# Performance work log

Hardware: AMD Instinct MI355X
Metric: run time of the kernel (lower is better)

## Reference

```python
import jax, jax.numpy as jnp
import numpy as np

S, N, H, E, V = 64, 256, 1024, 256, 128  # seq_len, batch, hidden, embed, vocab
DIR = 2  # bidirectional encoder


def setup_inputs() -> dict:
    key = jax.random.key(0)
    ks = jax.random.split(key, 16)
    sd = lambda fan: 1.0 / np.sqrt(fan)
    inp = {
        'x': jax.random.randint(ks[0], (N,), 0, V),
        'encoder_states': jax.random.normal(ks[1], (S, N, DIR * H), dtype=jnp.float32),
        'hidden': jax.random.normal(ks[2], (2, N, H), dtype=jnp.float32),
        'cell': jnp.zeros((2, N, H), dtype=jnp.float32),
        'emb': jax.random.normal(ks[3], (V, E), dtype=jnp.float32),
        'U_w': jax.random.normal(ks[4], (H, DIR * H), dtype=jnp.float32) * sd(DIR * H),
        'U_b': jnp.zeros((H,), jnp.float32),
        'W_w': jax.random.normal(ks[5], (H, H), dtype=jnp.float32) * sd(H),
        'W_b': jnp.zeros((H,), jnp.float32),
        'attn_w': jax.random.normal(ks[6], (1, H), dtype=jnp.float32) * sd(H),
        'attn_b': jnp.zeros((1,), jnp.float32),
        'W_ih0': jax.random.normal(ks[7], (3 * H, DIR * H + E), dtype=jnp.float32) * sd(H),
        'W_hh0': jax.random.normal(ks[8], (3 * H, H), dtype=jnp.float32) * sd(H),
        'b_ih0': jnp.zeros((3 * H,), jnp.float32),
        'b_hh0': jnp.zeros((3 * H,), jnp.float32),
        'W_ih1': jax.random.normal(ks[9], (3 * H, H), dtype=jnp.float32) * sd(H),
        'W_hh1': jax.random.normal(ks[10], (3 * H, H), dtype=jnp.float32) * sd(H),
        'b_ih1': jnp.zeros((3 * H,), jnp.float32),
        'b_hh1': jnp.zeros((3 * H,), jnp.float32),
        'fc_w': jax.random.normal(ks[11], (V, H), dtype=jnp.float32) * sd(H),
        'fc_b': jnp.zeros((V,), jnp.float32),
    }
    return inp


def _gru_cell(x, h, W_ih, W_hh, b_ih, b_hh):
    # PyTorch GRU cell math. x:(N,Din), h:(N,H) -> (N,H)
    gi = x @ W_ih.T + b_ih
    gh = h @ W_hh.T + b_hh
    ir, iz, i_n = jnp.split(gi, 3, axis=-1)
    hr, hz, h_n = jnp.split(gh, 3, axis=-1)
    r = jax.nn.sigmoid(ir + hr)
    z = jax.nn.sigmoid(iz + hz)
    n = jnp.tanh(i_n + r * h_n)
    return (1.0 - z) * n + z * h


def reference(x, encoder_states, hidden, cell, emb, U_w, U_b, W_w, W_b,
              attn_w, attn_b, W_ih0, W_hh0, b_ih0, b_hh0,
              W_ih1, W_hh1, b_ih1, b_hh1, fc_w, fc_b):
    # embedding (dropout is identity at inference)
    emb_x = emb[x]                                   # (N, E)
    # additive (Bahdanau) attention
    u = jnp.einsum('snd,hd->snh', encoder_states, U_w) + U_b   # (S,N,H)
    w = hidden[-1] @ W_w.T + W_b                                # (N,H)
    energy = jnp.tanh(u + w[None]) @ attn_w.T + attn_b          # (S,N,1)
    attention = jax.nn.softmax(energy, axis=0)                  # softmax over seq dim
    context = jnp.einsum('sn,snd->nd', attention[..., 0], encoder_states)  # (N, 2H)
    rnn_input = jnp.concatenate([context, emb_x], axis=-1)      # (N, 2H+E)
    # 2-layer single-step GRU (inter-layer dropout = identity at inference)
    h0 = _gru_cell(rnn_input, hidden[0], W_ih0, W_hh0, b_ih0, b_hh0)
    h1 = _gru_cell(h0, hidden[1], W_ih1, W_hh1, b_ih1, b_hh1)
    hidden_new = jnp.stack([h0, h1], axis=0)                    # (2, N, H)
    predictions = h1 @ fc_w.T + fc_b                            # (N, V)
    return predictions, hidden_new, attention
```

## Files before the change

kernel.cpp:

```cpp
#include <hip/hip_runtime.h>
#include <stdint.h>

typedef __attribute__((ext_vector_type(8))) short bf16x8;
typedef __attribute__((ext_vector_type(4))) float f32x4;
typedef __attribute__((ext_vector_type(8))) int i32x8;

#define DEVI __device__ __forceinline__

DEVI unsigned short f2bf(float f) {
    union { float f; uint32_t u; } v; v.f = f;
    uint32_t r = v.u + 0x7FFFu + ((v.u >> 16) & 1u);
    return (unsigned short)(r >> 16);
}
DEVI float bf2f(unsigned short h) {
    union { uint32_t u; float f; } v; v.u = ((uint32_t)h) << 16;
    return v.f;
}
DEVI bf16x8 pack8(float4 a, float4 b) {
    bf16x8 o;
    o[0]=(short)f2bf(a.x); o[1]=(short)f2bf(a.y); o[2]=(short)f2bf(a.z); o[3]=(short)f2bf(a.w);
    o[4]=(short)f2bf(b.x); o[5]=(short)f2bf(b.y); o[6]=(short)f2bf(b.z); o[7]=(short)f2bf(b.w);
    return o;
}

DEVI unsigned char f2e4m3(float x) {
    union { float f; uint32_t u; } v; v.f = x;
    uint32_t sign = (v.u >> 24) & 0x80u;
    v.u &= 0x7FFFFFFFu;
    if (v.f >= 464.f) return (unsigned char)(sign | 0x7Eu);
    if (v.f < 0.0009765625f) return (unsigned char)sign;
    uint32_t e = v.u >> 23;
    float q = __builtin_rintf(v.f * 512.f);
    uint32_t ms = (uint32_t)q;
    uint32_t subres = sign | (ms >= 8u ? 0x08u : ms);
    uint32_t r = v.u + 0x7FFFFu + ((v.u >> 20) & 1u);
    uint32_t er = r >> 23;
    uint32_t normres = (er > 135u) ? (sign | 0x7Eu)
                                   : (sign | ((er - 120u) << 3) | ((r >> 20) & 7u));
    return (unsigned char)((e < 121u) ? subres : normres);
}

DEVI float e4m3f(unsigned char u) {
    union { uint32_t u; float f; } v;
    v.u = (((uint32_t)u & 0x80u) << 24) | (((uint32_t)u & 0x7Fu) << 20);
    return v.f * 0x1p120f;
}

#define GLOAD_LDS16(gsrc, ldst) \
    __builtin_amdgcn_global_load_lds((__attribute__((address_space(1))) void*)(gsrc), \
                                     (__attribute__((address_space(3))) void*)(ldst), 16, 0, 0)

#define BARR asm volatile("s_barrier" ::: "memory")
#define WAITV(n) asm volatile("s_waitcnt vmcnt(" #n ")" ::: "memory")

__global__ void k_prep(const float* __restrict__ es, const float* __restrict__ U_w,
                       const float* __restrict__ W_w, const float* __restrict__ fc_w,
                       const float* __restrict__ hidden,
                       const float* __restrict__ Wih0, const float* __restrict__ Whh0,
                       const float* __restrict__ Wih1, const float* __restrict__ Whh1,
                       unsigned char* __restrict__ ES_F8, unsigned char* __restrict__ UW_F8,
                       unsigned short* __restrict__ WW_BF, unsigned short* __restrict__ FCW_BF,
                       unsigned short* __restrict__ A0, unsigned short* __restrict__ A1,
                       unsigned short* __restrict__ H1B,
                       unsigned short* __restrict__ B0, unsigned short* __restrict__ B1) {
    int i = blockIdx.x * blockDim.x + threadIdx.x;
    const int S0 = 4194304, S1 = S0 + 262144, S2 = S1 + 131072, S3 = S2 + 16384;
    const int S4 = S3 + 32768, S5 = S4 + 1703936, S6 = S5 + 1048576;
    if (i < S0) {
        const float4* s = (const float4*)(es + (size_t)i * 8);
        float4 a = s[0], b = s[1];
        float vv[8] = {a.x, a.y, a.z, a.w, b.x, b.y, b.z, b.w};
        unsigned long long p8 = 0;
        #pragma unroll
        for (int k = 0; k < 8; ++k) p8 |= (unsigned long long)f2e4m3(vv[k]) << (8 * k);
        *(unsigned long long*)(ES_F8 + (size_t)i * 8) = p8;
    } else if (i < S1) {
        int j = i - S0;
        const float4* s = (const float4*)(U_w + (size_t)j * 8);
        float4 a = s[0], b = s[1];
        float vv[8] = {a.x, a.y, a.z, a.w, b.x, b.y, b.z, b.w};
        unsigned long long p8 = 0;
        #pragma unroll
        for (int k = 0; k < 8; ++k) p8 |= (unsigned long long)f2e4m3(vv[k] * 16.f) << (8 * k);
        *(unsigned long long*)(UW_F8 + (size_t)j * 8) = p8;
    } else if (i < S2) {
        int j = i - S1;
        const float4* s = (const float4*)(W_w + (size_t)j * 8);
        *(bf16x8*)(WW_BF + (size_t)j * 8) = pack8(s[0], s[1]);
    } else if (i < S3) {
        int j = i - S2;
        const float4* s = (const float4*)(fc_w + (size_t)j * 8);
        *(bf16x8*)(FCW_BF + (size_t)j * 8) = pack8(s[0], s[1]);
    } else if (i < S4) {
        int j = i - S3;
        int n = j >> 7, e0 = (j & 127) * 8;
        const float4* p0 = (const float4*)(hidden + (size_t)n * 1024 + e0);
        const float4* p1 = (const float4*)(hidden + 262144 + (size_t)n * 1024 + e0);
        bf16x8 o0 = pack8(p0[0], p0[1]);
        bf16x8 o1 = pack8(p1[0], p1[1]);
        *(bf16x8*)(A0 + (size_t)n * 3328 + 2304 + e0) = o0;
        *(bf16x8*)(A1 + (size_t)n * 2048 + 1024 + e0) = o1;
        *(bf16x8*)(H1B + (size_t)n * 1024 + e0) = o1;
    } else if (i < S5) {
        unsigned j = (unsigned)(i - S4);
        unsigned r = j / 416u;
        int kc = (int)(j - r * 416u) * 8;
        const float* src = nullptr;
        if (r < 2048)      src = (kc < 2304) ? (Wih0 + (size_t)r * 2304 + kc)
                                             : (Whh0 + (size_t)r * 1024 + (kc - 2304));
        else if (r < 3072) { if (kc < 2304)  src = Wih0 + (size_t)r * 2304 + kc; }
        else               { if (kc >= 2304) src = Whh0 + (size_t)(r - 1024) * 1024 + (kc - 2304); }
        bf16x8 o;
        if (src) { const float4* s4 = (const float4*)src; o = pack8(s4[0], s4[1]); }
        else     { for (int k = 0; k < 8; ++k) o[k] = 0; }
        *(bf16x8*)(B0 + (size_t)r * 3328 + kc) = o;
    } else if (i < S6) {
        int j = i - S5;
        int r = j >> 8;
        int kc = (j & 255) * 8;
        const float* src = nullptr;
        if (r < 2048)      src = (kc < 1024) ? (Wih1 + (size_t)r * 1024 + kc)
                                             : (Whh1 + (size_t)r * 1024 + (kc - 1024));
        else if (r < 3072) { if (kc < 1024)  src = Wih1 + (size_t)r * 1024 + kc; }
        else               { if (kc >= 1024) src = Whh1 + (size_t)(r - 1024) * 1024 + (kc - 1024); }
        bf16x8 o;
        if (src) { const float4* s4 = (const float4*)src; o = pack8(s4[0], s4[1]); }
        else     { for (int k = 0; k < 8; ++k) o[k] = 0; }
        *(bf16x8*)(B1 + (size_t)r * 2048 + kc) = o;
    }
}

__global__ __launch_bounds__(256) void gemm_bt_sk2(
        const unsigned short* __restrict__ A, const unsigned short* __restrict__ B,
        float* __restrict__ Cpart, int K, int ksl) {
    __shared__ __align__(16) char lds[65536];
    const int NTT = ksl >> 6;

    const int t = threadIdx.x;
    const int w = t >> 6, lane = t & 63;
    const int wm = w >> 1, wn = w & 1;
    const int lg = lane >> 4, r16 = lane & 15;
    const int z = blockIdx.z;
    const int nbx = gridDim.x;
    const int N = nbx * 128, M = gridDim.y * 128;

    int d = blockIdx.y * nbx + blockIdx.x;
    int f = d;
    int nwg = nbx * gridDim.y;
    if ((nwg & 7) == 0) { int cpx = nwg >> 3; f = (d & 7) * cpx + (d >> 3); }
    const int bx = f % nbx, by = f / nbx;
    const int row0 = by * 128, col0 = bx * 128;

    const unsigned short* gsrc[8];
    unsigned lodst[8];
    #pragma unroll
    for (int q = 0; q < 8; ++q) {
        int isB = q >> 2, rq = q & 3;
        int row = rq * 32 + w * 8 + (lane >> 3);
        int slot = (lane & 7) ^ (lane >> 3);
        gsrc[q] = (isB ? B + (size_t)(col0 + row) * K
                       : A + (size_t)(row0 + row) * K) + (size_t)z * ksl + slot * 8;
        lodst[q] = (unsigned)(isB * 16384 + (rq * 32 + w * 8) * 128);
    }

#define STAGE(T) do { \
    char* lp_ = lds + ((T) & 1) * 32768; \
    _Pragma("unroll") \
    for (int q_ = 0; q_ < 8; ++q_) \
        GLOAD_LDS16(gsrc[q_] + (size_t)(T) * 64, lp_ + lodst[q_]); \
} while (0)

    const unsigned swz = (unsigned)((r16 & 7) << 4);
    unsigned aoff[4], boff[4];
    #pragma unroll
    for (int m = 0; m < 4; ++m)
        aoff[m] = ((unsigned)((wm * 64 + m * 16 + r16) * 128 + lg * 16)) ^ swz;
    #pragma unroll
    for (int n = 0; n < 4; ++n)
        boff[n] = 16384u + (((unsigned)((wn * 64 + n * 16 + r16) * 128 + lg * 16)) ^ swz);

    f32x4 acc[4][4];
    #pragma unroll
    for (int m = 0; m < 4; ++m)
        #pragma unroll
        for (int n = 0; n < 4; ++n)
            #pragma unroll
            for (int q = 0; q < 4; ++q) acc[m][n][q] = 0.0f;

    STAGE(0);
    #pragma unroll 1
    for (int tt = 0; tt < NTT; ++tt) {
        if (tt + 1 < NTT) { STAGE(tt + 1); WAITV(8); }
        else              { WAITV(0); }
        BARR;
        const char* lp = lds + (tt & 1) * 32768;
        #pragma unroll
        for (int kk = 0; kk < 2; ++kk) {
            bf16x8 afr[4], bfr[4];
            #pragma unroll
            for (int n = 0; n < 4; ++n) bfr[n] = *(const bf16x8*)(lp + (boff[n] ^ (kk << 6)));
            #pragma unroll
            for (int m = 0; m < 4; ++m) afr[m] = *(const bf16x8*)(lp + (aoff[m] ^ (kk << 6)));
            #pragma unroll
            for (int m = 0; m < 4; ++m)
                #pragma unroll
                for (int n = 0; n < 4; ++n)
                    acc[m][n] = __builtin_amdgcn_mfma_f32_16x16x32_bf16(
                        afr[m], bfr[n], acc[m][n], 0, 0, 0);
        }
        BARR;
    }
#undef STAGE

    float* Cz = Cpart + (size_t)z * (size_t)M * N;
    #pragma unroll
    for (int m = 0; m < 4; ++m)
        #pragma unroll
        for (int n = 0; n < 4; ++n)
            #pragma unroll
            for (int q = 0; q < 4; ++q) {
                int row = row0 + wm * 64 + m * 16 + lg * 4 + q;
                int col = col0 + wn * 64 + n * 16 + r16;
                Cz[(size_t)row * N + col] = acc[m][n][q];
            }
}

__global__ __launch_bounds__(256) void gemm_energy128_f8(
        const unsigned char* __restrict__ A, const unsigned char* __restrict__ B,
        const float* __restrict__ attn_w, const float* __restrict__ U_b,
        const float* __restrict__ W_b, const float* __restrict__ WP,
        float* __restrict__ e_part) {
    const int NTT = 16;
    __shared__ __align__(16) char lds[65536];

    const int t = threadIdx.x;
    const int w = t >> 6, lane = t & 63;
    const int wm = w >> 1, wn = w & 1;
    const int lg = lane >> 4, r16 = lane & 15;

    int d = blockIdx.y * gridDim.x + blockIdx.x;
    int f = (d & 7) * 128 + (d >> 3);
    const int bx = f & 7, by = f >> 3;
    const int row0 = by * 128, col0 = bx * 128;

    const unsigned char* gsrc[8];
    unsigned lodst[8];
    #pragma unroll
    for (int q = 0; q < 8; ++q) {
        int isB = q >> 2, rq = q & 3;
        int row = rq * 32 + w * 8 + (lane >> 3);
        int slot = (lane & 7) ^ (lane >> 3);
        gsrc[q] = (isB ? B + (size_t)(col0 + row) * 2048
                       : A + (size_t)(row0 + row) * 2048) + slot * 16;
        lodst[q] = (unsigned)(isB * 16384 + (rq * 32 + w * 8) * 128);
    }

#define STAGE(T) do { \
    char* lp_ = lds + ((T) & 1) * 32768; \
    _Pragma("unroll") \
    for (int q_ = 0; q_ < 8; ++q_) \
        GLOAD_LDS16(gsrc[q_] + (size_t)(T) * 128, lp_ + lodst[q_]); \
} while (0)

    unsigned s16[2];
    #pragma unroll
    for (int sel = 0; sel < 2; ++sel)
        s16[sel] = (unsigned)(((sel * 4 + lg) ^ (r16 & 7)) << 4);
    unsigned arow[4], brow[4];
    #pragma unroll
    for (int m = 0; m < 4; ++m) arow[m] = (unsigned)((wm * 64 + m * 16 + r16) * 128);
    #pragma unroll
    for (int n = 0; n < 4; ++n) brow[n] = 16384u + (unsigned)((wn * 64 + n * 16 + r16) * 128);

    f32x4 acc[4][4];
    #pragma unroll
    for (int m = 0; m < 4; ++m)
        #pragma unroll
        for (int n = 0; n < 4; ++n)
            #pragma unroll
            for (int q = 0; q < 4; ++q) acc[m][n][q] = 0.0f;

    STAGE(0);
    #pragma unroll 1
    for (int tt = 0; tt < NTT; ++tt) {
        if (tt + 1 < NTT) { STAGE(tt + 1); WAITV(8); }
        else              { WAITV(0); }
        BARR;
        const char* lp = lds + (tt & 1) * 32768;
        i32x8 a8[4], b8[4];
        #pragma unroll
        for (int n = 0; n < 4; ++n) {
            int4 lo = *(const int4*)(lp + brow[n] + s16[0]);
            int4 hi = *(const int4*)(lp + brow[n] + s16[1]);
            b8[n] = (i32x8){lo.x, lo.y, lo.z, lo.w, hi.x, hi.y, hi.z, hi.w};
        }
        #pragma unroll
        for (int m = 0; m < 4; ++m) {
            int4 lo = *(const int4*)(lp + arow[m] + s16[0]);
            int4 hi = *(const int4*)(lp + arow[m] + s16[1]);
            a8[m] = (i32x8){lo.x, lo.y, lo.z, lo.w, hi.x, hi.y, hi.z, hi.w};
        }
        #pragma unroll
        for (int m = 0; m < 4; ++m)
            #pragma unroll
            for (int n = 0; n < 4; ++n)
                acc[m][n] = __builtin_amdgcn_mfma_scale_f32_16x16x128_f8f6f4(
                    a8[m], b8[n], acc[m][n], 0, 0,
                    0, 0x7F7F7F7F, 0, 0x7F7F7F7F);
        BARR;
    }
#undef STAGE

    float aw[4], ub[4];
    #pragma unroll
    for (int n = 0; n < 4; ++n) {
        int col = col0 + wn * 64 + n * 16 + r16;
        aw[n] = attn_w[col];
        ub[n] = U_b[col] + W_b[col];
    }
    #pragma unroll
    for (int m = 0; m < 4; ++m)
        #pragma unroll
        for (int q = 0; q < 4; ++q) {
            int row = row0 + wm * 64 + m * 16 + lg * 4 + q;
            const float* wrow = WP + (size_t)(row & 255) * 1024;
            float e = 0.f;
            #pragma unroll
            for (int n = 0; n < 4; ++n) {
                int col = col0 + wn * 64 + n * 16 + r16;
                float wv = wrow[col] + wrow[262144 + col] + wrow[524288 + col] + wrow[786432 + col];
                float cc = acc[m][n][q] * 0.0625f + ub[n] + wv;
                float ex = __expf(2.f * cc);
                e += aw[n] * (1.f - 2.f / (ex + 1.f));
            }
            e += __shfl_xor(e, 1); e += __shfl_xor(e, 2);
            e += __shfl_xor(e, 4); e += __shfl_xor(e, 8);
            if (r16 == 0) e_part[(size_t)row * 16 + bx * 2 + wn] = e;
        }
}

__global__ __launch_bounds__(256) void k_softctx(
        const unsigned char* __restrict__ es8, const float* __restrict__ e_part,
        const float* __restrict__ emb, const int* __restrict__ x,
        float* __restrict__ attn_out, unsigned short* __restrict__ A0) {
    int n = blockIdx.x, t = threadIdx.x;
    __shared__ float as_[64];
    __shared__ float ev[64];
    {
        int s = t >> 2;
        const float* p = e_part + ((size_t)(s * 256 + n)) * 16 + (t & 3) * 4;
        float v = p[0] + p[1] + p[2] + p[3];
        v += __shfl_xor(v, 1); v += __shfl_xor(v, 2);
        if ((t & 3) == 0) ev[s] = v;
        __syncthreads();
        if (t < 64) {
            float e = ev[t];
            float mx = e;
            #pragma unroll
            for (int o = 1; o < 64; o <<= 1) mx = fmaxf(mx, __shfl_xor(mx, o));
            float ee = __expf(e - mx);
            float sum = ee;
            #pragma unroll
            for (int o = 1; o < 64; o <<= 1) sum += __shfl_xor(sum, o);
            float a = ee / sum;
            as_[t] = a;
            attn_out[t * 256 + n] = a;
        }
        __syncthreads();
    }
    float acc[8];
    #pragma unroll
    for (int k = 0; k < 8; ++k) acc[k] = 0.f;
    const unsigned char* base = es8 + (size_t)n * 2048 + t * 8;
    for (int s = 0; s < 64; ++s) {
        unsigned long long v = *(const unsigned long long*)(base + (size_t)s * 524288);
        float a = as_[s];
        #pragma unroll
        for (int k = 0; k < 8; ++k)
            acc[k] += a * e4m3f((unsigned char)(v >> (8 * k)));
    }
    bf16x8 o;
    #pragma unroll
    for (int k = 0; k < 8; ++k) o[k] = (short)f2bf(acc[k]);
    *(bf16x8*)(A0 + (size_t)n * 3328 + t * 8) = o;
    if (t < 32) {
        const float4* e4 = (const float4*)(emb + (size_t)x[n] * 256 + t * 8);
        *(bf16x8*)(A0 + (size_t)n * 3328 + 2048 + t * 8) = pack8(e4[0], e4[1]);
    }
}

__global__ void k_gru(const float* __restrict__ g, const float* __restrict__ b_ih,
                      const float* __restrict__ b_hh, const float* __restrict__ h_in,
                      float* __restrict__ h_out, unsigned short* __restrict__ a_dst,
                      int dst_pitch) {
    int i = blockIdx.x * blockDim.x + threadIdx.x;
    int n = i >> 10, e = i & 1023;
    const float* gn = g + (size_t)n * 4096;
    float rr = 0.f, zz = 0.f, in_ = 0.f, hn_ = 0.f;
    #pragma unroll
    for (int z = 0; z < 4; ++z) {
        const float* gz = gn + (size_t)z * 1048576;
        rr  += gz[e];
        zz  += gz[1024 + e];
        in_ += gz[2048 + e];
        hn_ += gz[3072 + e];
    }
    rr  += b_ih[e]        + b_hh[e];
    zz  += b_ih[1024 + e] + b_hh[1024 + e];
    in_ += b_ih[2048 + e];
    hn_ += b_hh[2048 + e];
    float r = 1.f / (1.f + __expf(-rr));
    float z = 1.f / (1.f + __expf(-zz));
    float ex = __expf(2.f * (in_ + r * hn_));
    float nn = 1.f - 2.f / (ex + 1.f);
    float h = h_in[i];
    float ho = (1.f - z) * nn + z * h;
    h_out[i] = ho;
    a_dst[(size_t)n * dst_pitch + e] = f2bf(ho);
}

__global__ void k_fcsum(const float* __restrict__ Fp, const float* __restrict__ fc_b,
                        float* __restrict__ outp) {
    int i = blockIdx.x * blockDim.x + threadIdx.x;
    outp[i] = Fp[i] + Fp[32768 + i] + Fp[65536 + i] + Fp[98304 + i] + fc_b[i & 127];
}


extern "C" void kernel_launch(void* const* d_in, const int* in_sizes, int n_in,
                              void* d_out, int out_size, void* d_ws, size_t ws_size,
                              hipStream_t stream) {
    const int*   x      = (const int*)  d_in[0];
    const float* es     = (const float*)d_in[1];
    const float* hidden = (const float*)d_in[2];
    const float* emb    = (const float*)d_in[4];
    const float* U_w    = (const float*)d_in[5];
    const float* U_b    = (const float*)d_in[6];
    const float* W_w    = (const float*)d_in[7];
    const float* W_b    = (const float*)d_in[8];
    const float* attn_w = (const float*)d_in[9];
    const float* W_ih0  = (const float*)d_in[11];
    const float* W_hh0  = (const float*)d_in[12];
    const float* b_ih0  = (const float*)d_in[13];
    const float* b_hh0  = (const float*)d_in[14];
    const float* W_ih1  = (const float*)d_in[15];
    const float* W_hh1  = (const float*)d_in[16];
    const float* b_ih1  = (const float*)d_in[17];
    const float* b_hh1  = (const float*)d_in[18];
    const float* fc_w   = (const float*)d_in[19];
    const float* fc_b   = (const float*)d_in[20];

    float* out        = (float*)d_out;
    float* out_pred   = out;
    float* out_hidden = out + 32768;
    float* out_attn   = out + 32768 + 524288;

    char* ws = (char*)d_ws;
    size_t off = 0;
    auto alloc = [&](size_t bytes) { char* p = ws + off; off += (bytes + 255) & ~(size_t)255; return p; };
    unsigned char*  ES_F8  = (unsigned char*) alloc((size_t)16384 * 2048);
    unsigned char*  UW_F8  = (unsigned char*) alloc((size_t)1024 * 2048);
    unsigned short* WW_BF  = (unsigned short*)alloc((size_t)1024 * 1024 * 2);
    unsigned short* FCW_BF = (unsigned short*)alloc((size_t)128 * 1024 * 2);
    unsigned short* H1_BF  = (unsigned short*)alloc((size_t)256 * 1024 * 2);
    unsigned short* B0     = (unsigned short*)alloc((size_t)4096 * 3328 * 2);
    unsigned short* B1     = (unsigned short*)alloc((size_t)4096 * 2048 * 2);
    unsigned short* A0     = (unsigned short*)alloc((size_t)256 * 3328 * 2);
    unsigned short* A1     = (unsigned short*)alloc((size_t)256 * 2048 * 2);
    unsigned short* FCA    = (unsigned short*)alloc((size_t)256 * 1024 * 2);
    float* EPART = (float*)alloc((size_t)16384 * 16 * 4);
    float* WP    = (float*)alloc((size_t)4 * 256 * 1024 * 4);
    float* G0P   = (float*)alloc((size_t)4 * 256 * 4096 * 4);
    float* FCP   = WP;
    float* G1P   = G0P;

    k_prep<<<28864, 256, 0, stream>>>(es, U_w, W_w, fc_w, hidden, W_ih0, W_hh0, W_ih1, W_hh1,
                                      ES_F8, UW_F8, WW_BF, FCW_BF, A0, A1, H1_BF, B0, B1);
    gemm_bt_sk2<<<dim3(8, 2, 4), 256, 0, stream>>>(H1_BF, WW_BF, WP, 1024, 256);
    gemm_energy128_f8<<<dim3(8, 128), 256, 0, stream>>>(ES_F8, UW_F8, attn_w, U_b, W_b, WP, EPART);
    k_softctx<<<256, 256, 0, stream>>>(ES_F8, EPART, emb, x, out_attn, A0);
    gemm_bt_sk2<<<dim3(32, 2, 4), 256, 0, stream>>>(A0, B0, G0P, 3328, 832);
    k_gru<<<1024, 256, 0, stream>>>(G0P, b_ih0, b_hh0, hidden, out_hidden, A1, 2048);
    gemm_bt_sk2<<<dim3(32, 2, 4), 256, 0, stream>>>(A1, B1, G1P, 2048, 512);
    k_gru<<<1024, 256, 0, stream>>>(G1P, b_ih1, b_hh1, hidden + 262144, out_hidden + 262144, FCA, 1024);
    gemm_bt_sk2<<<dim3(1, 2, 4), 256, 0, stream>>>(FCA, FCW_BF, FCP, 1024, 256);
    k_fcsum<<<128, 256, 0, stream>>>(FCP, fc_b, out_pred);
}
```

Before: 166.5 us.

## Move GRU weight bf16 packing from prep kernel into energy GEMM epilogue

The conversion of the GRU weight matrices (B0, B1) to bf16 moves out of the big k_prep kernel and into the tail of the fp8 energy GEMM kernel. Each of the 1024 energy blocks converts a slice of 2688 chunks of 8 values after its epilogue. The aim is to hide the bandwidth-bound weight conversion behind the compute-bound GEMM and shrink the prep launch. The risk is that the energy kernel gets longer, carries more registers, and its memory traffic competes with the GEMM loads.

Result: slower. 174.4 us (+4.8%).

```diff
diff --git a/kernel.cpp b/kernel.cpp
--- a/kernel.cpp
+++ b/kernel.cpp
@@ -56,16 +56,13 @@
 __global__ void k_prep(const float* __restrict__ es, const float* __restrict__ U_w,
                        const float* __restrict__ W_w, const float* __restrict__ fc_w,
                        const float* __restrict__ hidden,
-                       const float* __restrict__ Wih0, const float* __restrict__ Whh0,
-                       const float* __restrict__ Wih1, const float* __restrict__ Whh1,
                        unsigned char* __restrict__ ES_F8, unsigned char* __restrict__ UW_F8,
                        unsigned short* __restrict__ WW_BF, unsigned short* __restrict__ FCW_BF,
                        unsigned short* __restrict__ A0, unsigned short* __restrict__ A1,
-                       unsigned short* __restrict__ H1B,
-                       unsigned short* __restrict__ B0, unsigned short* __restrict__ B1) {
+                       unsigned short* __restrict__ H1B) {
     int i = blockIdx.x * blockDim.x + threadIdx.x;
     const int S0 = 4194304, S1 = S0 + 262144, S2 = S1 + 131072, S3 = S2 + 16384;
-    const int S4 = S3 + 32768, S5 = S4 + 1703936, S6 = S5 + 1048576;
+    const int S4 = S3 + 32768;
     if (i < S0) {
         const float4* s = (const float4*)(es + (size_t)i * 8);
         float4 a = s[0], b = s[1];
@@ -101,32 +98,6 @@
         *(bf16x8*)(A0 + (size_t)n * 3328 + 2304 + e0) = o0;
         *(bf16x8*)(A1 + (size_t)n * 2048 + 1024 + e0) = o1;
         *(bf16x8*)(H1B + (size_t)n * 1024 + e0) = o1;
-    } else if (i < S5) {
-        unsigned j = (unsigned)(i - S4);
-        unsigned r = j / 416u;
-        int kc = (int)(j - r * 416u) * 8;
-        const float* src = nullptr;
-        if (r < 2048)      src = (kc < 2304) ? (Wih0 + (size_t)r * 2304 + kc)
-                                             : (Whh0 + (size_t)r * 1024 + (kc - 2304));
-        else if (r < 3072) { if (kc < 2304)  src = Wih0 + (size_t)r * 2304 + kc; }
-        else               { if (kc >= 2304) src = Whh0 + (size_t)(r - 1024) * 1024 + (kc - 2304); }
-        bf16x8 o;
-        if (src) { const float4* s4 = (const float4*)src; o = pack8(s4[0], s4[1]); }
-        else     { for (int k = 0; k < 8; ++k) o[k] = 0; }
-        *(bf16x8*)(B0 + (size_t)r * 3328 + kc) = o;
-    } else if (i < S6) {
-        int j = i - S5;
-        int r = j >> 8;
-        int kc = (j & 255) * 8;
-        const float* src = nullptr;
-        if (r < 2048)      src = (kc < 1024) ? (Wih1 + (size_t)r * 1024 + kc)
-                                             : (Whh1 + (size_t)r * 1024 + (kc - 1024));
-        else if (r < 3072) { if (kc < 1024)  src = Wih1 + (size_t)r * 1024 + kc; }
-        else               { if (kc >= 1024) src = Whh1 + (size_t)(r - 1024) * 1024 + (kc - 1024); }
-        bf16x8 o;
-        if (src) { const float4* s4 = (const float4*)src; o = pack8(s4[0], s4[1]); }
-        else     { for (int k = 0; k < 8; ++k) o[k] = 0; }
-        *(bf16x8*)(B1 + (size_t)r * 2048 + kc) = o;
     }
 }
 
@@ -229,6 +200,9 @@
         const unsigned char* __restrict__ A, const unsigned char* __restrict__ B,
         const float* __restrict__ attn_w, const float* __restrict__ U_b,
         const float* __restrict__ W_b, const float* __restrict__ WP,
+        const float* __restrict__ Wih0, const float* __restrict__ Whh0,
+        const float* __restrict__ Wih1, const float* __restrict__ Whh1,
+        unsigned short* __restrict__ B0, unsigned short* __restrict__ B1,
         float* __restrict__ e_part) {
     const int NTT = 16;
     __shared__ __align__(16) char lds[65536];
@@ -337,6 +311,42 @@
             e += __shfl_xor(e, 4); e += __shfl_xor(e, 8);
             if (r16 == 0) e_part[(size_t)row * 16 + bx * 2 + wn] = e;
         }
+
+    {
+        int cbase = d * 2688 + t;
+        #pragma unroll 1
+        for (int c = 0; c < 11; ++c) {
+            int off_in_blk = t + c * 256;
+            if (off_in_blk >= 2688) break;
+            int j = cbase + c * 256;
+            if (j < 1703936) {
+                unsigned r = (unsigned)j / 416u;
+                int kc = (int)((unsigned)j - r * 416u) * 8;
+                const float* src = nullptr;
+                if (r < 2048)      src = (kc < 2304) ? (Wih0 + (size_t)r * 2304 + kc)
+                                                     : (Whh0 + (size_t)r * 1024 + (kc - 2304));
+                else if (r < 3072) { if (kc < 2304)  src = Wih0 + (size_t)r * 2304 + kc; }
+                else               { if (kc >= 2304) src = Whh0 + (size_t)(r - 1024) * 1024 + (kc - 2304); }
+                bf16x8 o;
+                if (src) { const float4* s4 = (const float4*)src; o = pack8(s4[0], s4[1]); }
+                else     { for (int k = 0; k < 8; ++k) o[k] = 0; }
+                *(bf16x8*)(B0 + (size_t)r * 3328 + kc) = o;
+            } else {
+                int j2 = j - 1703936;
+                int r = j2 >> 8;
+                int kc = (j2 & 255) * 8;
+                const float* src = nullptr;
+                if (r < 2048)      src = (kc < 1024) ? (Wih1 + (size_t)r * 1024 + kc)
+                                                     : (Whh1 + (size_t)r * 1024 + (kc - 1024));
+                else if (r < 3072) { if (kc < 1024)  src = Wih1 + (size_t)r * 1024 + kc; }
+                else               { if (kc >= 1024) src = Whh1 + (size_t)(r - 1024) * 1024 + (kc - 1024); }
+                bf16x8 o;
+                if (src) { const float4* s4 = (const float4*)src; o = pack8(s4[0], s4[1]); }
+                else     { for (int k = 0; k < 8; ++k) o[k] = 0; }
+                *(bf16x8*)(B1 + (size_t)r * 2048 + kc) = o;
+            }
+        }
+    }
 }
 
 __global__ __launch_bounds__(256) void k_softctx(
@@ -473,10 +483,11 @@
     float* FCP   = WP;
     float* G1P   = G0P;
 
-    k_prep<<<28864, 256, 0, stream>>>(es, U_w, W_w, fc_w, hidden, W_ih0, W_hh0, W_ih1, W_hh1,
-                                      ES_F8, UW_F8, WW_BF, FCW_BF, A0, A1, H1_BF, B0, B1);
+    k_prep<<<18112, 256, 0, stream>>>(es, U_w, W_w, fc_w, hidden,
+                                      ES_F8, UW_F8, WW_BF, FCW_BF, A0, A1, H1_BF);
     gemm_bt_sk2<<<dim3(8, 2, 4), 256, 0, stream>>>(H1_BF, WW_BF, WP, 1024, 256);
-    gemm_energy128_f8<<<dim3(8, 128), 256, 0, stream>>>(ES_F8, UW_F8, attn_w, U_b, W_b, WP, EPART);
+    gemm_energy128_f8<<<dim3(8, 128), 256, 0, stream>>>(ES_F8, UW_F8, attn_w, U_b, W_b, WP,
+                                                        W_ih0, W_hh0, W_ih1, W_hh1, B0, B1, EPART);
     k_softctx<<<256, 256, 0, stream>>>(ES_F8, EPART, emb, x, out_attn, A0);
     gemm_bt_sk2<<<dim3(32, 2, 4), 256, 0, stream>>>(A0, B0, G0P, 3328, 832);
     k_gru<<<1024, 256, 0, stream>>>(G0P, b_ih0, b_hh0, hidden, out_hidden, A1, 2048);
```
